# Optimization experiments

Measured on AMD Instinct MI355X. Metric: run time of the kernel, lower is better.

## Reference

```python
import jax, jax.numpy as jnp
import numpy as np

N_NODES = 50000
N_EDGES = 800000
DIM = 128
N_GRAPHS = 64
HEADS = 4
SCALE = (DIM // HEADS) ** -0.5
EPS = 1e-5
SLOPE = 0.01  # torch LeakyReLU default


def setup_inputs() -> dict:
    key = jax.random.key(0)
    ks = iter(jax.random.split(key, 48))
    def nrm(shape, s):
        return jax.random.normal(next(ks), shape, dtype=jnp.float32) * s
    inp = {
        "xA": nrm((N_NODES, DIM), 1.0),
        "xB": nrm((N_NODES, DIM), 1.0),
        "edge_index_A": jax.random.randint(next(ks), (2, N_EDGES), 0, N_NODES),
        "edge_index_B": jax.random.randint(next(ks), (2, N_EDGES), 0, N_NODES),
        # contiguous equal-size graph assignment (sorted, covers all B graphs)
        "batch_A": (jnp.arange(N_NODES) * N_GRAPHS) // N_NODES,
        "batch_B": (jnp.arange(N_NODES) * N_GRAPHS) // N_NODES,
    }
    s = DIM ** -0.5
    for name, shape in [("WA1", (DIM, DIM)), ("WA2", (DIM, DIM)),
                        ("WB1", (DIM, DIM)), ("WB2", (DIM, DIM)),
                        ("Wq", (DIM, DIM)), ("Wk", (DIM, DIM)),
                        ("Wv", (DIM, DIM)), ("Wo", (DIM, DIM)),
                        ("Wf1", (DIM, 2 * DIM)), ("Wf2", (2 * DIM, DIM)),
                        ("Wl1", (2 * DIM, DIM)), ("Wl2", (DIM, 1))]:
        inp[name] = nrm(shape, s)
    for name, shape in [("bA1", (DIM,)), ("bA2", (DIM,)), ("bB1", (DIM,)), ("bB2", (DIM,)),
                        ("bq", (DIM,)), ("bk", (DIM,)), ("bv", (DIM,)), ("bo", (DIM,)),
                        ("bf1", (2 * DIM,)), ("bf2", (DIM,)), ("bl1", (DIM,)), ("bl2", (1,))]:
        inp[name] = jnp.zeros(shape, jnp.float32)
    inp["g1"] = jnp.ones((DIM,), jnp.float32)
    inp["be1"] = jnp.zeros((DIM,), jnp.float32)
    inp["g2"] = jnp.ones((DIM,), jnp.float32)
    inp["be2"] = jnp.zeros((DIM,), jnp.float32)
    return inp


def _gcn(x, W, b, src, dst):
    # PyG GCNConv: XW, add self-loops, sym D^-1/2 (A+I) D^-1/2, scatter to dst, + bias
    h = x @ W
    deg = jax.ops.segment_sum(jnp.ones(src.shape, h.dtype), dst, N_NODES) + 1.0
    inv = jax.lax.rsqrt(deg)
    agg = jax.ops.segment_sum(h[src] * (inv[src] * inv[dst])[:, None], dst, N_NODES)
    return agg + h * (inv * inv)[:, None] + b  # self-loop term: norm_i^2 * h_i


def _encoder(x, edge_index, W1, b1, W2, b2):
    src, dst = edge_index[0], edge_index[1]
    h = jax.nn.leaky_relu(_gcn(x, W1, b1, src, dst), SLOPE)
    return _gcn(h, W2, b2, src, dst)  # dropout is identity in eval mode


def _pool(x, batch):
    s = jax.ops.segment_sum(x, batch, N_GRAPHS)
    c = jax.ops.segment_sum(jnp.ones((x.shape[0],), x.dtype), batch, N_GRAPHS)
    return s / c[:, None]


def _ln(x, g, b):
    m = x.mean(-1, keepdims=True)
    v = ((x - m) ** 2).mean(-1, keepdims=True)
    return (x - m) * jax.lax.rsqrt(v + EPS) * g + b


def reference(xA, xB, edge_index_A, edge_index_B, batch_A, batch_B,
              WA1, bA1, WA2, bA2, WB1, bB1, WB2, bB2,
              Wq, bq, Wk, bk, Wv, bv, Wo, bo,
              g1, be1, Wf1, bf1, Wf2, bf2, g2, be2,
              Wl1, bl1, Wl2, bl2):

    def cross(x_q, x_kv):
        Q = (x_q @ Wq + bq).reshape(-1, HEADS, DIM // HEADS)
        K = (x_kv @ Wk + bk).reshape(-1, HEADS, DIM // HEADS)
        V = (x_kv @ Wv + bv).reshape(-1, HEADS, DIM // HEADS)
        attn = jax.nn.softmax(jnp.einsum('qhd,khd->hqk', Q, K) * SCALE, axis=-1)
        out = jnp.einsum('hqk,khd->qhd', attn, V).reshape(x_q.shape[0], DIM)
        return out @ Wo + bo

    def block(x_q, x_kv):  # shared-weight CrossAttentionBlock (used both directions)
        x = _ln(x_q + cross(x_q, x_kv), g1, be1)
        ff = jax.nn.leaky_relu(x @ Wf1 + bf1, SLOPE) @ Wf2 + bf2
        return _ln(x + ff, g2, be2)

    gA = _encoder(xA, edge_index_A, WA1, bA1, WA2, bA2)
    gB = _encoder(xB, edge_index_B, WB1, bB1, WB2, bB2)
    hA = _pool(gA, batch_A)
    hB = _pool(gB, batch_B)
    hA_att = block(hA, hB)
    hB_att = block(hB, hA)
    h = jnp.concatenate([hA_att, hB_att], axis=-1)  # [B, 2*DIM]
    h = jax.nn.relu(h @ Wl1 + bl1)
    return h @ Wl2 + bl2  # [B, 1]
```

## Files before the change

### kernel.cpp

```cpp
#include <hip/hip_runtime.h>

#define N_NODESC 50000
#define N_EDGESC 800000
#define DIMC 128
#define NGC 64
#define HDC 32
#define SLOPEF 0.01f
#define EPSF 1e-5f
#define SCALEF 0.17677669529663687f

#define NBUK 782
#define KBLK 50
#define EPB 16000
#define GG 782
#define AG 12500

typedef __attribute__((ext_vector_type(8))) short bf16x8;
typedef __attribute__((ext_vector_type(4))) float f32x4;
typedef __attribute__((ext_vector_type(2))) float f32x2;

static __device__ __forceinline__ unsigned short f2bf(float f) {
  unsigned u = __float_as_uint(f);
  u = u + 0x7FFFu + ((u >> 16) & 1u);
  return (unsigned short)(u >> 16);
}
static __device__ __forceinline__ float bf2f(unsigned short h) {
  return __uint_as_float(((unsigned)h) << 16);
}

#if defined(__has_builtin)
#if __has_builtin(__builtin_amdgcn_cvt_pk_f32_fp8) && __has_builtin(__builtin_amdgcn_cvt_pk_fp8_f32)
#define HW_FP8 1
#endif
#endif
#ifndef HW_FP8
#define HW_FP8 0
#endif

static __device__ __forceinline__ unsigned enc_fp8(float x) {
  unsigned u = __float_as_uint(x);
  unsigned s = (u >> 24) & 0x80u;
  unsigned mag = u & 0x7FFFFFFFu;
  if (mag >= 0x43E00000u) return s | 0x7Eu;
  unsigned r = mag + 0x7FFFFu + ((mag >> 20) & 1u);
  int e8 = (int)(r >> 23) - 120;
  if (e8 <= 0) {
    float ax = __uint_as_float(mag);
    int m = (int)(ax * 512.0f + 0.5f);
    if (m > 7) m = 7;
    return s | (unsigned)m;
  }
  return s | ((unsigned)e8 << 3) | ((r >> 20) & 7u);
}
static __device__ __forceinline__ float dec_fp8(unsigned b) {
  unsigned em = b & 0x7Fu;
  float mag = (em >= 8) ? __uint_as_float((em << 20) + 0x3C000000u)
                        : (float)em * 0.001953125f;
  return (b & 0x80u) ? -mag : mag;
}
static __device__ __forceinline__ unsigned pk_fp8x4(float a, float b, float c, float d) {
#if HW_FP8
  int v = 0;
  v = __builtin_amdgcn_cvt_pk_fp8_f32(a, b, v, false);
  v = __builtin_amdgcn_cvt_pk_fp8_f32(c, d, v, true);
  return (unsigned)v;
#else
  return enc_fp8(a) | (enc_fp8(b) << 8) | (enc_fp8(c) << 16) | (enc_fp8(d) << 24);
#endif
}
static __device__ __forceinline__ float4 upk_fp8x4(unsigned v) {
#if HW_FP8
  f32x2 lo = __builtin_amdgcn_cvt_pk_f32_fp8((int)v, false);
  f32x2 hi = __builtin_amdgcn_cvt_pk_f32_fp8((int)v, true);
  return make_float4(lo[0], lo[1], hi[0], hi[1]);
#else
  return make_float4(dec_fp8(v & 0xFF), dec_fp8((v >> 8) & 0xFF),
                     dec_fp8((v >> 16) & 0xFF), dec_fp8(v >> 24));
#endif
}

__global__ __launch_bounds__(1024) void kbhist2(const int* __restrict__ eiA, const int* __restrict__ eiB,
                                                int* __restrict__ hist) {
  __shared__ int lh[NBUK];
  int side = blockIdx.x / KBLK, blk = blockIdx.x % KBLK;
  const int* ei = side ? eiB : eiA;
  int* hout = hist + side * KBLK * NBUK;
  int t = threadIdx.x;
  for (int i = t; i < NBUK; i += 1024) lh[i] = 0;
  __syncthreads();
  int e0 = blk * EPB;
  for (int e = e0 + t; e < e0 + EPB; e += 1024) {
    int d = ei[N_EDGESC + e];
    atomicAdd(&lh[d >> 6], 1);
  }
  __syncthreads();
  for (int i = t; i < NBUK; i += 1024) hout[blk * NBUK + i] = lh[i];
}

__global__ __launch_bounds__(1024) void kbscan2(const int* __restrict__ hist, int* __restrict__ bbase,
                                                int* __restrict__ bucket_base) {
  __shared__ int sd[1024];
  int side = blockIdx.x;
  const int* h = hist + side * KBLK * NBUK;
  int* bb = bbase + side * KBLK * NBUK;
  int* bub = bucket_base + side * (NBUK + 1);
  int t = threadIdx.x;
  int tot = 0;
  if (t < NBUK) {
    for (int k = 0; k < KBLK; ++k) tot += h[k * NBUK + t];
  }
  sd[t] = tot;
  __syncthreads();
  for (int off = 1; off < 1024; off <<= 1) {
    int u = (t >= off) ? sd[t - off] : 0;
    __syncthreads();
    sd[t] += u;
    __syncthreads();
  }
  if (t < NBUK) {
    int run = sd[t] - tot;
    bub[t] = run;
    for (int k = 0; k < KBLK; ++k) {
      bb[k * NBUK + t] = run;
      run += h[k * NBUK + t];
    }
  }
  if (t == 0) bub[NBUK] = N_EDGESC;
}

__global__ __launch_bounds__(1024) void kbin2(const int* __restrict__ eiA, const int* __restrict__ eiB,
                                              const int* __restrict__ bbase, unsigned* __restrict__ packed) {
  __shared__ int cur[NBUK];
  int side = blockIdx.x / KBLK, blk = blockIdx.x % KBLK;
  const int* ei = side ? eiB : eiA;
  const int* bb = bbase + side * KBLK * NBUK;
  unsigned* pk = packed + (size_t)side * N_EDGESC;
  int t = threadIdx.x;
  for (int i = t; i < NBUK; i += 1024) cur[i] = bb[blk * NBUK + i];
  __syncthreads();
  int e0 = blk * EPB;
  for (int e = e0 + t; e < e0 + EPB; e += 1024) {
    int s = ei[e];
    int d = ei[N_EDGESC + e];
    int b = d >> 6;
    int pos = atomicAdd(&cur[b], 1);
    pk[pos] = (unsigned)s | ((unsigned)(d & 63) << 16);
  }
}

__global__ __launch_bounds__(256) void kcsr2(const unsigned* __restrict__ packed, const int* __restrict__ bucket_base,
                                             unsigned short* __restrict__ csr16, int* __restrict__ rowptr,
                                             float* __restrict__ inv) {
  __shared__ int h64[64], o64[64], c64[64];
  int side = blockIdx.x / NBUK, b = blockIdx.x % NBUK;
  const unsigned* pk = packed + (size_t)side * N_EDGESC;
  const int* bub = bucket_base + side * (NBUK + 1);
  unsigned short* cs = csr16 + (size_t)side * N_EDGESC;
  int* rp = rowptr + side * (N_NODESC + 1);
  float* iv = inv + side * N_NODESC;
  int t = threadIdx.x;
  int beg = bub[b], end = bub[b + 1];
  if (t < 64) h64[t] = 0;
  __syncthreads();
  for (int e = beg + t; e < end; e += 256) atomicAdd(&h64[pk[e] >> 16], 1);
  __syncthreads();
  if (t == 0) {
    int run = 0;
    for (int j = 0; j < 64; ++j) { o64[j] = run; run += h64[j]; }
  }
  __syncthreads();
  if (t < 64) c64[t] = o64[t];
  __syncthreads();
  for (int e = beg + t; e < end; e += 256) {
    unsigned p = pk[e];
    int pos = atomicAdd(&c64[p >> 16], 1);
    cs[beg + pos] = (unsigned short)(p & 0xFFFFu);
  }
  if (t < 64) {
    int node = b * 64 + t;
    if (node < N_NODESC) {
      rp[node] = beg + o64[t];
      iv[node] = rsqrtf((float)h64[t] + 1.0f);
    }
  }
  if (b == NBUK - 1 && t == 0) rp[N_NODESC] = N_EDGESC;
}

__global__ __launch_bounds__(256) void wconv(const float* __restrict__ W0, const float* __restrict__ W1,
                                             const float* __restrict__ W2, const float* __restrict__ W3,
                                             unsigned short* __restrict__ Wt) {
  int m = blockIdx.x >> 4;
  int idx = (blockIdx.x & 15) * 256 + threadIdx.x;
  int fs = idx >> 6, lane = idx & 63;
  int ks = fs >> 3, nf = fs & 7;
  int n = nf * 16 + (lane & 15);
  int k0 = ks * 32 + (lane >> 4) * 8;
  const float* W = (m == 0) ? W0 : (m == 1) ? W1 : (m == 2) ? W2 : W3;
  unsigned short* hi = Wt + (size_t)m * 128 * 512 + (size_t)(fs * 2) * 512 + lane * 8;
  bf16x8 vh, vl;
#pragma unroll
  for (int j = 0; j < 8; ++j) {
    float a = W[(k0 + j) * DIMC + n];
    unsigned short h = f2bf(a);
    vh[j] = (short)h;
    vl[j] = (short)f2bf(a - bf2f(h));
  }
  *(bf16x8*)hi = vh;
  *(bf16x8*)(hi + 512) = vl;
}

static __device__ __forceinline__ void epi_store_fp8(const unsigned short* lds, unsigned* Y, int lb) {
  int tr = threadIdx.x >> 2, q = threadIdx.x & 3;
  int grow = lb * 64 + tr;
  if (grow >= N_NODESC) return;
#pragma unroll
  for (int i = 0; i < 8; ++i) {
    int col = (q + 4 * i) * 4;
    ushort4 v = *(const ushort4*)&lds[tr * 136 + col];
    unsigned pk = pk_fp8x4(bf2f(v.x), bf2f(v.y), bf2f(v.z), bf2f(v.w));
    Y[(size_t)grow * 32 + q + 4 * i] = pk;
  }
}

__global__ __launch_bounds__(256) void gemm_l1(const float* __restrict__ xA, const float* __restrict__ xB,
                                               const unsigned short* __restrict__ Wt, const float* __restrict__ inv,
                                               unsigned* __restrict__ H) {
  __shared__ unsigned short lds[64 * 136];
  int side = blockIdx.x / GG, lb = blockIdx.x % GG;
  const float* X = side ? xB : xA;
  const unsigned short* Wm = Wt + (size_t)(side * 2) * 128 * 512;
  const float* iv = inv + side * N_NODESC;
  unsigned* Y = H + (size_t)side * N_NODESC * 32;
  int wave = threadIdx.x >> 6, lane = threadIdx.x & 63;
  int l15 = lane & 15, kb = lane >> 4;
  int row0 = lb * 64 + wave * 16;
  int rA = row0 + l15;
  const bool valid = rA < N_NODESC;
  f32x4 acc[8];
#pragma unroll
  for (int nf = 0; nf < 8; ++nf) acc[nf] = 0.f;
#pragma unroll
  for (int ks = 0; ks < 4; ++ks) {
    int kbase = ks * 32 + kb * 8;
    bf16x8 a;
    if (valid) {
      const float* xp = &X[(size_t)rA * DIMC + kbase];
      float4 x0 = *(const float4*)xp;
      float4 x1 = *(const float4*)(xp + 4);
      a[0] = (short)f2bf(x0.x); a[1] = (short)f2bf(x0.y);
      a[2] = (short)f2bf(x0.z); a[3] = (short)f2bf(x0.w);
      a[4] = (short)f2bf(x1.x); a[5] = (short)f2bf(x1.y);
      a[6] = (short)f2bf(x1.z); a[7] = (short)f2bf(x1.w);
    } else {
      a = (short)0;
    }
    const unsigned short* wp = Wm + (size_t)(ks * 16) * 512 + lane * 8;
#pragma unroll
    for (int nf = 0; nf < 8; ++nf) {
      bf16x8 bh = *(const bf16x8*)(wp + (nf * 2) * 512);
      bf16x8 bl = *(const bf16x8*)(wp + (nf * 2 + 1) * 512);
      acc[nf] = __builtin_amdgcn_mfma_f32_16x16x32_bf16(a, bh, acc[nf], 0, 0, 0);
      acc[nf] = __builtin_amdgcn_mfma_f32_16x16x32_bf16(a, bl, acc[nf], 0, 0, 0);
    }
  }
  int lrow = wave * 16 + kb * 4;
#pragma unroll
  for (int r = 0; r < 4; ++r) {
    int rr = row0 + kb * 4 + r;
    float s = (rr < N_NODESC) ? iv[rr] * 16.0f : 0.f;
#pragma unroll
    for (int nf = 0; nf < 8; ++nf) {
      lds[(lrow + r) * 136 + nf * 16 + l15] = f2bf(acc[nf][r] * s);
    }
  }
  __syncthreads();
  epi_store_fp8(lds, Y, lb);
}

__global__ __launch_bounds__(256) void gemm_l2(const unsigned short* __restrict__ Gb,
                                               const unsigned short* __restrict__ Wt, const float* __restrict__ inv,
                                               unsigned* __restrict__ H) {
  __shared__ unsigned short lds[64 * 136];
  int side = blockIdx.x / GG, lb = blockIdx.x % GG;
  const unsigned short* X = Gb + (size_t)side * N_NODESC * DIMC;
  const unsigned short* Wm = Wt + (size_t)(side * 2 + 1) * 128 * 512;
  const float* iv = inv + side * N_NODESC;
  unsigned* Y = H + (size_t)side * N_NODESC * 32;
  int wave = threadIdx.x >> 6, lane = threadIdx.x & 63;
  int l15 = lane & 15, kb = lane >> 4;
  int row0 = lb * 64 + wave * 16;
  int rA = row0 + l15;
  const bool valid = rA < N_NODESC;
  f32x4 acc[8];
#pragma unroll
  for (int nf = 0; nf < 8; ++nf) acc[nf] = 0.f;
#pragma unroll
  for (int ks = 0; ks < 4; ++ks) {
    int kbase = ks * 32 + kb * 8;
    bf16x8 a;
    if (valid) {
      a = *(const bf16x8*)&X[(size_t)rA * DIMC + kbase];
    } else {
      a = (short)0;
    }
    const unsigned short* wp = Wm + (size_t)(ks * 16) * 512 + lane * 8;
#pragma unroll
    for (int nf = 0; nf < 8; ++nf) {
      bf16x8 bh = *(const bf16x8*)(wp + (nf * 2) * 512);
      bf16x8 bl = *(const bf16x8*)(wp + (nf * 2 + 1) * 512);
      acc[nf] = __builtin_amdgcn_mfma_f32_16x16x32_bf16(a, bh, acc[nf], 0, 0, 0);
      acc[nf] = __builtin_amdgcn_mfma_f32_16x16x32_bf16(a, bl, acc[nf], 0, 0, 0);
    }
  }
  int lrow = wave * 16 + kb * 4;
#pragma unroll
  for (int r = 0; r < 4; ++r) {
    int rr = row0 + kb * 4 + r;
    float s = (rr < N_NODESC) ? iv[rr] * 16.0f : 0.f;
#pragma unroll
    for (int nf = 0; nf < 8; ++nf) {
      lds[(lrow + r) * 136 + nf * 16 + l15] = f2bf(acc[nf][r] * s);
    }
  }
  __syncthreads();
  epi_store_fp8(lds, Y, lb);
}

__global__ __launch_bounds__(256) void agg12(const unsigned* __restrict__ H, const float* __restrict__ inv,
                                             const int* __restrict__ rowptr, const unsigned short* __restrict__ csr16,
                                             const float* __restrict__ biasA, const float* __restrict__ biasB,
                                             unsigned short* __restrict__ G, int do_relu) {
  int side = blockIdx.x / AG, lb = blockIdx.x % AG;
  int node = lb * 4 + (threadIdx.x >> 6);
  if (node >= N_NODESC) return;
  const unsigned* Hp = H + (size_t)side * N_NODESC * 32;
  const float* iv = inv + side * N_NODESC;
  const int* rp = rowptr + side * (N_NODESC + 1);
  const unsigned short* csr = csr16 + (size_t)side * N_EDGESC;
  const float* bias = side ? biasB : biasA;
  unsigned short* out = G + (size_t)side * N_NODESC * DIMC;
  int lane = threadIdx.x & 63;
  int ug = lane & 31;
  int slot = lane >> 5;
  int beg = rp[node], end = rp[node + 1];
  float4 acc = make_float4(0.f, 0.f, 0.f, 0.f);
  int e = beg;
  for (; e + 8 <= end; e += 8) {
    int s0 = csr[e + slot];
    int s1 = csr[e + 2 + slot];
    int s2 = csr[e + 4 + slot];
    int s3 = csr[e + 6 + slot];
    unsigned u0 = Hp[(size_t)s0 * 32 + ug];
    unsigned u1 = Hp[(size_t)s1 * 32 + ug];
    unsigned u2 = Hp[(size_t)s2 * 32 + ug];
    unsigned u3 = Hp[(size_t)s3 * 32 + ug];
    float4 v0 = upk_fp8x4(u0);
    float4 v1 = upk_fp8x4(u1);
    float4 v2 = upk_fp8x4(u2);
    float4 v3 = upk_fp8x4(u3);
    acc.x += (v0.x + v1.x) + (v2.x + v3.x);
    acc.y += (v0.y + v1.y) + (v2.y + v3.y);
    acc.z += (v0.z + v1.z) + (v2.z + v3.z);
    acc.w += (v0.w + v1.w) + (v2.w + v3.w);
  }
  for (int t = e + slot; t < end; t += 2) {
    int s = csr[t];
    float4 v = upk_fp8x4(Hp[(size_t)s * 32 + ug]);
    acc.x += v.x; acc.y += v.y; acc.z += v.z; acc.w += v.w;
  }
  acc.x += __shfl_xor(acc.x, 32, 64);
  acc.y += __shfl_xor(acc.y, 32, 64);
  acc.z += __shfl_xor(acc.z, 32, 64);
  acc.w += __shfl_xor(acc.w, 32, 64);
  if (slot == 0) {
    float4 sv = upk_fp8x4(Hp[(size_t)node * 32 + ug]);
    float sc = iv[node] * 0.0625f;
    const float* bp = &bias[ug * 4];
    float4 b = *(const float4*)bp;
    float4 o;
    o.x = (acc.x + sv.x) * sc + b.x;
    o.y = (acc.y + sv.y) * sc + b.y;
    o.z = (acc.z + sv.z) * sc + b.z;
    o.w = (acc.w + sv.w) * sc + b.w;
    if (do_relu) {
      o.x = (o.x > 0.f) ? o.x : SLOPEF * o.x;
      o.y = (o.y > 0.f) ? o.y : SLOPEF * o.y;
      o.z = (o.z > 0.f) ? o.z : SLOPEF * o.z;
      o.w = (o.w > 0.f) ? o.w : SLOPEF * o.w;
    }
    ushort4 ob;
    ob.x = f2bf(o.x); ob.y = f2bf(o.y); ob.z = f2bf(o.z); ob.w = f2bf(o.w);
    *(ushort4*)&out[(size_t)node * DIMC + ug * 4] = ob;
  }
}

__global__ __launch_bounds__(128) void pool2(const unsigned short* __restrict__ G,
                                             const int* __restrict__ batA, const int* __restrict__ batB,
                                             float* __restrict__ psA, float* __restrict__ psB,
                                             int* __restrict__ pcA, int* __restrict__ pcB) {
  int side = blockIdx.x / GG, lb = blockIdx.x % GG;
  const unsigned short* g = G + (size_t)side * N_NODESC * DIMC;
  const int* batch = side ? batB : batA;
  float* psum = side ? psB : psA;
  int* pcnt = side ? pcB : pcA;
  int t = threadIdx.x;
  int n0 = lb * 64;
  int nend = min(n0 + 64, N_NODESC);
  int cur = batch[n0];
  float acc = 0.f;
  int c = 0;
  for (int n = n0; n < nend; ++n) {
    int b = batch[n];
    if (b != cur) {
      atomicAdd(&psum[cur * DIMC + t], acc);
      if (t == 0) atomicAdd(&pcnt[cur], c);
      acc = 0.f;
      c = 0;
      cur = b;
    }
    acc += bf2f(g[(size_t)n * DIMC + t]);
    c += 1;
  }
  atomicAdd(&psum[cur * DIMC + t], acc);
  if (t == 0) atomicAdd(&pcnt[cur], c);
}

__global__ __launch_bounds__(128) void mean_kernel(const float* __restrict__ psA, const int* __restrict__ pcA,
                                                   const float* __restrict__ psB, const int* __restrict__ pcB,
                                                   float* __restrict__ hA, float* __restrict__ hB) {
  int dir = blockIdx.x >> 6, g = blockIdx.x & 63, t = threadIdx.x;
  const float* ps = dir ? psB : psA;
  const int* pc = dir ? pcB : pcA;
  float* h = dir ? hB : hA;
  h[g * DIMC + t] = ps[g * DIMC + t] / (float)max(pc[g], 1);
}

__global__ __launch_bounds__(128) void qkv_kernel(const float* __restrict__ hA, const float* __restrict__ hB,
                                                  const float* __restrict__ Wq, const float* __restrict__ bq,
                                                  const float* __restrict__ Wk, const float* __restrict__ bk,
                                                  const float* __restrict__ Wv, const float* __restrict__ bv,
                                                  float* __restrict__ Q0, float* __restrict__ K0, float* __restrict__ V0,
                                                  float* __restrict__ Q1, float* __restrict__ K1, float* __restrict__ V1) {
  __shared__ float xs[DIMC];
  int task = blockIdx.x >> 6, r = blockIdx.x & 63, t = threadIdx.x;
  const float *X, *W, *b;
  float* Y;
  switch (task) {
    case 0: X = hA; W = Wq; b = bq; Y = Q0; break;
    case 1: X = hB; W = Wk; b = bk; Y = K0; break;
    case 2: X = hB; W = Wv; b = bv; Y = V0; break;
    case 3: X = hB; W = Wq; b = bq; Y = Q1; break;
    case 4: X = hA; W = Wk; b = bk; Y = K1; break;
    default: X = hA; W = Wv; b = bv; Y = V1; break;
  }
  xs[t] = X[r * DIMC + t];
  __syncthreads();
  float acc = b[t];
  for (int k = 0; k < DIMC; ++k) acc += xs[k] * W[k * DIMC + t];
  Y[r * DIMC + t] = acc;
}

__global__ __launch_bounds__(64) void attn_kernel(const float* __restrict__ Q0, const float* __restrict__ K0,
                                                  const float* __restrict__ V0, const float* __restrict__ Q1,
                                                  const float* __restrict__ K1, const float* __restrict__ V1,
                                                  float* __restrict__ O0, float* __restrict__ O1) {
  __shared__ float ps[64];
  int b = blockIdx.x;
  int dir = b >> 8, h = (b >> 6) & 3, q = b & 63;
  const float* Q = dir ? Q1 : Q0;
  const float* K = dir ? K1 : K0;
  const float* V = dir ? V1 : V0;
  float* O = dir ? O1 : O0;
  int k = threadIdx.x;
  const float* qp = Q + q * DIMC + h * HDC;
  const float* kp = K + k * DIMC + h * HDC;
  float s = 0.f;
#pragma unroll
  for (int d = 0; d < HDC; ++d) s += qp[d] * kp[d];
  s *= SCALEF;
  float m = s;
#pragma unroll
  for (int off = 32; off >= 1; off >>= 1) m = fmaxf(m, __shfl_xor(m, off, 64));
  float p = __expf(s - m);
  float sum = p;
#pragma unroll
  for (int off = 32; off >= 1; off >>= 1) sum += __shfl_xor(sum, off, 64);
  p /= sum;
  ps[k] = p;
  __syncthreads();
  int half = k >> 5, d = k & 31;
  float acc = 0.f;
#pragma unroll
  for (int j = 0; j < 32; ++j) {
    int kk = half * 32 + j;
    acc += ps[kk] * V[kk * DIMC + h * HDC + d];
  }
  acc += __shfl_xor(acc, 32, 64);
  if (half == 0) O[q * DIMC + h * HDC + d] = acc;
}

__device__ inline float blk_sum128(float v, float* red) {
#pragma unroll
  for (int off = 32; off >= 1; off >>= 1) v += __shfl_xor(v, off, 64);
  if ((threadIdx.x & 63) == 0) red[threadIdx.x >> 6] = v;
  __syncthreads();
  float r = red[0] + red[1];
  __syncthreads();
  return r;
}

__global__ __launch_bounds__(128) void oln_kernel(const float* __restrict__ O0, const float* __restrict__ O1,
                                                  const float* __restrict__ hA, const float* __restrict__ hB,
                                                  const float* __restrict__ Wo, const float* __restrict__ bo,
                                                  const float* __restrict__ g1, const float* __restrict__ be1,
                                                  float* __restrict__ X0, float* __restrict__ X1) {
  __shared__ float os[DIMC];
  __shared__ float red[2];
  int dir = blockIdx.x >> 6, q = blockIdx.x & 63, t = threadIdx.x;
  const float* O = dir ? O1 : O0;
  const float* xq = dir ? hB : hA;
  float* Xo = dir ? X1 : X0;
  os[t] = O[q * DIMC + t];
  __syncthreads();
  float acc = bo[t] + xq[q * DIMC + t];
  for (int k = 0; k < DIMC; ++k) acc += os[k] * Wo[k * DIMC + t];
  float mean = blk_sum128(acc, red) * (1.f / DIMC);
  float d = acc - mean;
  float var = blk_sum128(d * d, red) * (1.f / DIMC);
  Xo[q * DIMC + t] = d * rsqrtf(var + EPSF) * g1[t] + be1[t];
}

__global__ __launch_bounds__(256) void ff1_kernel(const float* __restrict__ X0, const float* __restrict__ X1,
                                                  const float* __restrict__ Wf1, const float* __restrict__ bf1,
                                                  float* __restrict__ F0, float* __restrict__ F1) {
  __shared__ float xs[DIMC];
  int dir = blockIdx.x >> 6, q = blockIdx.x & 63, t = threadIdx.x;
  const float* X = dir ? X1 : X0;
  float* F = dir ? F1 : F0;
  if (t < DIMC) xs[t] = X[q * DIMC + t];
  __syncthreads();
  float acc = bf1[t];
  for (int k = 0; k < DIMC; ++k) acc += xs[k] * Wf1[k * 256 + t];
  acc = (acc > 0.f) ? acc : SLOPEF * acc;
  F[q * 256 + t] = acc;
}

__global__ __launch_bounds__(128) void ffln_kernel(const float* __restrict__ F0, const float* __restrict__ F1,
                                                   const float* __restrict__ X0, const float* __restrict__ X1,
                                                   const float* __restrict__ Wf2, const float* __restrict__ bf2,
                                                   const float* __restrict__ g2, const float* __restrict__ be2,
                                                   float* __restrict__ Y0, float* __restrict__ Y1) {
  __shared__ float fs[256];
  __shared__ float red[2];
  int dir = blockIdx.x >> 6, q = blockIdx.x & 63, t = threadIdx.x;
  const float* F = dir ? F1 : F0;
  const float* X = dir ? X1 : X0;
  float* Y = dir ? Y1 : Y0;
  fs[t] = F[q * 256 + t];
  fs[t + 128] = F[q * 256 + t + 128];
  __syncthreads();
  float acc = bf2[t] + X[q * DIMC + t];
  for (int k = 0; k < 256; ++k) acc += fs[k] * Wf2[k * DIMC + t];
  float mean = blk_sum128(acc, red) * (1.f / DIMC);
  float d = acc - mean;
  float var = blk_sum128(d * d, red) * (1.f / DIMC);
  Y[q * DIMC + t] = d * rsqrtf(var + EPSF) * g2[t] + be2[t];
}

__global__ __launch_bounds__(128) void head_kernel(const float* __restrict__ Y0, const float* __restrict__ Y1,
                                                   const float* __restrict__ Wl1, const float* __restrict__ bl1,
                                                   const float* __restrict__ Wl2, const float* __restrict__ bl2,
                                                   float* __restrict__ out) {
  __shared__ float cs[256];
  __shared__ float red[2];
  int g = blockIdx.x, t = threadIdx.x;
  cs[t] = Y0[g * DIMC + t];
  cs[t + 128] = Y1[g * DIMC + t];
  __syncthreads();
  float acc = bl1[t];
  for (int k = 0; k < 256; ++k) acc += cs[k] * Wl1[k * DIMC + t];
  acc = fmaxf(acc, 0.f);
  float s = blk_sum128(acc * Wl2[t], red);
  if (t == 0) out[g] = s + bl2[0];
}

extern "C" void kernel_launch(void* const* d_in, const int* in_sizes, int n_in,
                              void* d_out, int out_size, void* d_ws, size_t ws_size,
                              hipStream_t stream) {
  const float* xA = (const float*)d_in[0];
  const float* xB = (const float*)d_in[1];
  const int* eiA = (const int*)d_in[2];
  const int* eiB = (const int*)d_in[3];
  const int* batA = (const int*)d_in[4];
  const int* batB = (const int*)d_in[5];
  const float* WA1 = (const float*)d_in[6];
  const float* WA2 = (const float*)d_in[7];
  const float* WB1 = (const float*)d_in[8];
  const float* WB2 = (const float*)d_in[9];
  const float* Wq = (const float*)d_in[10];
  const float* Wk = (const float*)d_in[11];
  const float* Wv = (const float*)d_in[12];
  const float* Wo = (const float*)d_in[13];
  const float* Wf1 = (const float*)d_in[14];
  const float* Wf2 = (const float*)d_in[15];
  const float* Wl1 = (const float*)d_in[16];
  const float* Wl2 = (const float*)d_in[17];
  const float* bA1 = (const float*)d_in[18];
  const float* bA2 = (const float*)d_in[19];
  const float* bB1 = (const float*)d_in[20];
  const float* bB2 = (const float*)d_in[21];
  const float* bq = (const float*)d_in[22];
  const float* bk = (const float*)d_in[23];
  const float* bv = (const float*)d_in[24];
  const float* bo = (const float*)d_in[25];
  const float* bf1 = (const float*)d_in[26];
  const float* bf2 = (const float*)d_in[27];
  const float* bl1 = (const float*)d_in[28];
  const float* bl2 = (const float*)d_in[29];
  const float* g1 = (const float*)d_in[30];
  const float* be1 = (const float*)d_in[31];
  const float* g2 = (const float*)d_in[32];
  const float* be2 = (const float*)d_in[33];

  char* base = (char*)d_ws;
  size_t off = 0;
  auto alloc = [&](size_t bytes) -> char* {
    char* r = base + off;
    off += (bytes + 255) & ~(size_t)255;
    return r;
  };
  unsigned* h_buf = (unsigned*)alloc((size_t)2 * N_NODESC * 32 * 4);
  unsigned short* g_buf = (unsigned short*)alloc((size_t)2 * N_NODESC * DIMC * 2);
  unsigned* packed = (unsigned*)alloc((size_t)2 * N_EDGESC * 4);
  unsigned short* csr16 = (unsigned short*)alloc((size_t)2 * N_EDGESC * 2);
  int* rowptr = (int*)alloc((size_t)2 * (N_NODESC + 1) * 4);
  float* inv = (float*)alloc((size_t)2 * N_NODESC * 4);
  int* hist = (int*)alloc((size_t)2 * KBLK * NBUK * 4);
  int* bbase = (int*)alloc((size_t)2 * KBLK * NBUK * 4);
  int* bucket_base = (int*)alloc((size_t)2 * (NBUK + 1) * 4);
  unsigned short* wtbuf = (unsigned short*)alloc((size_t)4 * 128 * 512 * 2);
  size_t poff0 = off;
  float* psA = (float*)alloc(NGC * DIMC * 4);
  float* psB = (float*)alloc(NGC * DIMC * 4);
  int* pcA = (int*)alloc(NGC * 4);
  int* pcB = (int*)alloc(NGC * 4);
  size_t pbytes = off - poff0;
  float* mhA = (float*)alloc(NGC * DIMC * 4);
  float* mhB = (float*)alloc(NGC * DIMC * 4);
  float* Q0 = (float*)alloc(NGC * DIMC * 4);
  float* K0 = (float*)alloc(NGC * DIMC * 4);
  float* V0 = (float*)alloc(NGC * DIMC * 4);
  float* Q1 = (float*)alloc(NGC * DIMC * 4);
  float* K1 = (float*)alloc(NGC * DIMC * 4);
  float* V1 = (float*)alloc(NGC * DIMC * 4);
  float* O0 = (float*)alloc(NGC * DIMC * 4);
  float* O1 = (float*)alloc(NGC * DIMC * 4);
  float* X0 = (float*)alloc(NGC * DIMC * 4);
  float* X1 = (float*)alloc(NGC * DIMC * 4);
  float* F0 = (float*)alloc(NGC * 256 * 4);
  float* F1 = (float*)alloc(NGC * 256 * 4);
  float* Y0 = (float*)alloc(NGC * DIMC * 4);
  float* Y1 = (float*)alloc(NGC * DIMC * 4);

  hipMemsetAsync(base + poff0, 0, pbytes, stream);
  wconv<<<64, 256, 0, stream>>>(WA1, WA2, WB1, WB2, wtbuf);

  kbhist2<<<2 * KBLK, 1024, 0, stream>>>(eiA, eiB, hist);
  kbscan2<<<2, 1024, 0, stream>>>(hist, bbase, bucket_base);
  kbin2<<<2 * KBLK, 1024, 0, stream>>>(eiA, eiB, bbase, packed);
  kcsr2<<<2 * NBUK, 256, 0, stream>>>(packed, bucket_base, csr16, rowptr, inv);

  gemm_l1<<<2 * GG, 256, 0, stream>>>(xA, xB, wtbuf, inv, h_buf);
  agg12<<<2 * AG, 256, 0, stream>>>(h_buf, inv, rowptr, csr16, bA1, bB1, g_buf, 1);
  gemm_l2<<<2 * GG, 256, 0, stream>>>(g_buf, wtbuf, inv, h_buf);
  agg12<<<2 * AG, 256, 0, stream>>>(h_buf, inv, rowptr, csr16, bA2, bB2, g_buf, 0);
  pool2<<<2 * GG, 128, 0, stream>>>(g_buf, batA, batB, psA, psB, pcA, pcB);

  mean_kernel<<<128, 128, 0, stream>>>(psA, pcA, psB, pcB, mhA, mhB);
  qkv_kernel<<<384, 128, 0, stream>>>(mhA, mhB, Wq, bq, Wk, bk, Wv, bv, Q0, K0, V0, Q1, K1, V1);
  attn_kernel<<<512, 64, 0, stream>>>(Q0, K0, V0, Q1, K1, V1, O0, O1);
  oln_kernel<<<128, 128, 0, stream>>>(O0, O1, mhA, mhB, Wo, bo, g1, be1, X0, X1);
  ff1_kernel<<<128, 256, 0, stream>>>(X0, X1, Wf1, bf1, F0, F1);
  ffln_kernel<<<128, 128, 0, stream>>>(F0, F1, X0, X1, Wf2, bf2, g2, be2, Y0, Y1);
  head_kernel<<<64, 128, 0, stream>>>(Y0, Y1, Wl1, bl1, Wl2, bl2, (float*)d_out);
}
```

Measured before the change: 268.0 us.

## Widen aggregation loads to 8 bytes and fuse tail kernels

The GCN aggregation kernel now has each lane read a uint2 (8 fp8 values). Sixteen lanes cover one feature row, so four edges are gathered in parallel per wave, with a 16-edge unrolled loop and a two-step shuffle reduction. Separately, the small post-pool kernels are merged: mean with QKV, output projection/LN with FF1, and FF2/LN with the head. This cuts three launches and their global round-trips. The trade-off is more accumulator registers in the aggregation and a 256-thread block where half the threads idle during the Wo stage.

```diff
diff --git a/kernel.cpp b/kernel.cpp
--- a/kernel.cpp
+++ b/kernel.cpp
@@ -326,6 +326,13 @@
   epi_store_fp8(lds, Y, lb);
 }
 
+static __device__ __forceinline__ void addu2(float* acc, uint2 u) {
+  float4 a = upk_fp8x4(u.x);
+  float4 b = upk_fp8x4(u.y);
+  acc[0] += a.x; acc[1] += a.y; acc[2] += a.z; acc[3] += a.w;
+  acc[4] += b.x; acc[5] += b.y; acc[6] += b.z; acc[7] += b.w;
+}
+
 __global__ __launch_bounds__(256) void agg12(const unsigned* __restrict__ H, const float* __restrict__ inv,
                                              const int* __restrict__ rowptr, const unsigned short* __restrict__ csr16,
                                              const float* __restrict__ biasA, const float* __restrict__ biasB,
@@ -340,57 +347,60 @@
   const float* bias = side ? biasB : biasA;
   unsigned short* out = G + (size_t)side * N_NODESC * DIMC;
   int lane = threadIdx.x & 63;
-  int ug = lane & 31;
-  int slot = lane >> 5;
+  int g16 = lane & 15;
+  int ug2 = g16 * 2;
+  int slot = lane >> 4;
   int beg = rp[node], end = rp[node + 1];
-  float4 acc = make_float4(0.f, 0.f, 0.f, 0.f);
+  float acc[8];
+#pragma unroll
+  for (int j = 0; j < 8; ++j) acc[j] = 0.f;
   int e = beg;
-  for (; e + 8 <= end; e += 8) {
+  for (; e + 16 <= end; e += 16) {
     int s0 = csr[e + slot];
-    int s1 = csr[e + 2 + slot];
-    int s2 = csr[e + 4 + slot];
-    int s3 = csr[e + 6 + slot];
-    unsigned u0 = Hp[(size_t)s0 * 32 + ug];
-    unsigned u1 = Hp[(size_t)s1 * 32 + ug];
-    unsigned u2 = Hp[(size_t)s2 * 32 + ug];
-    unsigned u3 = Hp[(size_t)s3 * 32 + ug];
-    float4 v0 = upk_fp8x4(u0);
-    float4 v1 = upk_fp8x4(u1);
-    float4 v2 = upk_fp8x4(u2);
-    float4 v3 = upk_fp8x4(u3);
-    acc.x += (v0.x + v1.x) + (v2.x + v3.x);
-    acc.y += (v0.y + v1.y) + (v2.y + v3.y);
-    acc.z += (v0.z + v1.z) + (v2.z + v3.z);
-    acc.w += (v0.w + v1.w) + (v2.w + v3.w);
-  }
-  for (int t = e + slot; t < end; t += 2) {
-    int s = csr[t];
-    float4 v = upk_fp8x4(Hp[(size_t)s * 32 + ug]);
-    acc.x += v.x; acc.y += v.y; acc.z += v.z; acc.w += v.w;
-  }
-  acc.x += __shfl_xor(acc.x, 32, 64);
-  acc.y += __shfl_xor(acc.y, 32, 64);
-  acc.z += __shfl_xor(acc.z, 32, 64);
-  acc.w += __shfl_xor(acc.w, 32, 64);
+    int s1 = csr[e + 4 + slot];
+    int s2 = csr[e + 8 + slot];
+    int s3 = csr[e + 12 + slot];
+    uint2 u0 = *(const uint2*)&Hp[(size_t)s0 * 32 + ug2];
+    uint2 u1 = *(const uint2*)&Hp[(size_t)s1 * 32 + ug2];
+    uint2 u2 = *(const uint2*)&Hp[(size_t)s2 * 32 + ug2];
+    uint2 u3 = *(const uint2*)&Hp[(size_t)s3 * 32 + ug2];
+    addu2(acc, u0); addu2(acc, u1); addu2(acc, u2); addu2(acc, u3);
+  }
+  for (int t2 = e + slot; t2 < end; t2 += 4) {
+    uint2 u = *(const uint2*)&Hp[(size_t)csr[t2] * 32 + ug2];
+    addu2(acc, u);
+  }
+#pragma unroll
+  for (int j = 0; j < 8; ++j) {
+    acc[j] += __shfl_xor(acc[j], 16, 64);
+    acc[j] += __shfl_xor(acc[j], 32, 64);
+  }
   if (slot == 0) {
-    float4 sv = upk_fp8x4(Hp[(size_t)node * 32 + ug]);
+    uint2 su = *(const uint2*)&Hp[(size_t)node * 32 + ug2];
+    float4 sa = upk_fp8x4(su.x);
+    float4 sb = upk_fp8x4(su.y);
     float sc = iv[node] * 0.0625f;
-    const float* bp = &bias[ug * 4];
-    float4 b = *(const float4*)bp;
-    float4 o;
-    o.x = (acc.x + sv.x) * sc + b.x;
-    o.y = (acc.y + sv.y) * sc + b.y;
-    o.z = (acc.z + sv.z) * sc + b.z;
-    o.w = (acc.w + sv.w) * sc + b.w;
+    float4 b0 = *(const float4*)&bias[g16 * 8];
+    float4 b1 = *(const float4*)&bias[g16 * 8 + 4];
+    float o[8];
+    o[0] = (acc[0] + sa.x) * sc + b0.x;
+    o[1] = (acc[1] + sa.y) * sc + b0.y;
+    o[2] = (acc[2] + sa.z) * sc + b0.z;
+    o[3] = (acc[3] + sa.w) * sc + b0.w;
+    o[4] = (acc[4] + sb.x) * sc + b1.x;
+    o[5] = (acc[5] + sb.y) * sc + b1.y;
+    o[6] = (acc[6] + sb.z) * sc + b1.z;
+    o[7] = (acc[7] + sb.w) * sc + b1.w;
     if (do_relu) {
-      o.x = (o.x > 0.f) ? o.x : SLOPEF * o.x;
-      o.y = (o.y > 0.f) ? o.y : SLOPEF * o.y;
-      o.z = (o.z > 0.f) ? o.z : SLOPEF * o.z;
-      o.w = (o.w > 0.f) ? o.w : SLOPEF * o.w;
-    }
-    ushort4 ob;
-    ob.x = f2bf(o.x); ob.y = f2bf(o.y); ob.z = f2bf(o.z); ob.w = f2bf(o.w);
-    *(ushort4*)&out[(size_t)node * DIMC + ug * 4] = ob;
+#pragma unroll
+      for (int j = 0; j < 8; ++j) o[j] = (o[j] > 0.f) ? o[j] : SLOPEF * o[j];
+    }
+    uint4 w;
+    w.x = (unsigned)f2bf(o[0]) | ((unsigned)f2bf(o[1]) << 16);
+    w.y = (unsigned)f2bf(o[2]) | ((unsigned)f2bf(o[3]) << 16);
+    w.z = (unsigned)f2bf(o[4]) | ((unsigned)f2bf(o[5]) << 16);
+    w.w = (unsigned)f2bf(o[6]) | ((unsigned)f2bf(o[7]) << 16);
+    *(uint4*)&out[(size_t)node * DIMC + g16 * 8] = w;
   }
 }
 
@@ -425,35 +435,33 @@
   if (t == 0) atomicAdd(&pcnt[cur], c);
 }
 
-__global__ __launch_bounds__(128) void mean_kernel(const float* __restrict__ psA, const int* __restrict__ pcA,
-                                                   const float* __restrict__ psB, const int* __restrict__ pcB,
-                                                   float* __restrict__ hA, float* __restrict__ hB) {
-  int dir = blockIdx.x >> 6, g = blockIdx.x & 63, t = threadIdx.x;
-  const float* ps = dir ? psB : psA;
-  const int* pc = dir ? pcB : pcA;
-  float* h = dir ? hB : hA;
-  h[g * DIMC + t] = ps[g * DIMC + t] / (float)max(pc[g], 1);
-}
-
-__global__ __launch_bounds__(128) void qkv_kernel(const float* __restrict__ hA, const float* __restrict__ hB,
-                                                  const float* __restrict__ Wq, const float* __restrict__ bq,
-                                                  const float* __restrict__ Wk, const float* __restrict__ bk,
-                                                  const float* __restrict__ Wv, const float* __restrict__ bv,
-                                                  float* __restrict__ Q0, float* __restrict__ K0, float* __restrict__ V0,
-                                                  float* __restrict__ Q1, float* __restrict__ K1, float* __restrict__ V1) {
+__global__ __launch_bounds__(128) void meanqkv(const float* __restrict__ psA, const int* __restrict__ pcA,
+                                               const float* __restrict__ psB, const int* __restrict__ pcB,
+                                               const float* __restrict__ Wq, const float* __restrict__ bq,
+                                               const float* __restrict__ Wk, const float* __restrict__ bk,
+                                               const float* __restrict__ Wv, const float* __restrict__ bv,
+                                               float* __restrict__ mhA, float* __restrict__ mhB,
+                                               float* __restrict__ Q0, float* __restrict__ K0, float* __restrict__ V0,
+                                               float* __restrict__ Q1, float* __restrict__ K1, float* __restrict__ V1) {
   __shared__ float xs[DIMC];
   int task = blockIdx.x >> 6, r = blockIdx.x & 63, t = threadIdx.x;
-  const float *X, *W, *b;
+  bool sideA = (task == 0 || task == 4 || task == 5);
+  const float* ps = sideA ? psA : psB;
+  const int* pc = sideA ? pcA : pcB;
+  const float *W, *b;
   float* Y;
   switch (task) {
-    case 0: X = hA; W = Wq; b = bq; Y = Q0; break;
-    case 1: X = hB; W = Wk; b = bk; Y = K0; break;
-    case 2: X = hB; W = Wv; b = bv; Y = V0; break;
-    case 3: X = hB; W = Wq; b = bq; Y = Q1; break;
-    case 4: X = hA; W = Wk; b = bk; Y = K1; break;
-    default: X = hA; W = Wv; b = bv; Y = V1; break;
-  }
-  xs[t] = X[r * DIMC + t];
+    case 0: W = Wq; b = bq; Y = Q0; break;
+    case 1: W = Wk; b = bk; Y = K0; break;
+    case 2: W = Wv; b = bv; Y = V0; break;
+    case 3: W = Wq; b = bq; Y = Q1; break;
+    case 4: W = Wk; b = bk; Y = K1; break;
+    default: W = Wv; b = bv; Y = V1; break;
+  }
+  float xv = ps[r * DIMC + t] / (float)max(pc[r], 1);
+  xs[t] = xv;
+  if (task == 0) mhA[r * DIMC + t] = xv;
+  if (task == 3) mhB[r * DIMC + t] = xv;
   __syncthreads();
   float acc = b[t];
   for (int k = 0; k < DIMC; ++k) acc += xs[k] * W[k * DIMC + t];
@@ -509,74 +517,80 @@
   return r;
 }
 
-__global__ __launch_bounds__(128) void oln_kernel(const float* __restrict__ O0, const float* __restrict__ O1,
-                                                  const float* __restrict__ hA, const float* __restrict__ hB,
-                                                  const float* __restrict__ Wo, const float* __restrict__ bo,
-                                                  const float* __restrict__ g1, const float* __restrict__ be1,
-                                                  float* __restrict__ X0, float* __restrict__ X1) {
+__global__ __launch_bounds__(256) void olnff1(const float* __restrict__ O0, const float* __restrict__ O1,
+                                              const float* __restrict__ mhA, const float* __restrict__ mhB,
+                                              const float* __restrict__ Wo, const float* __restrict__ bo,
+                                              const float* __restrict__ g1, const float* __restrict__ be1,
+                                              const float* __restrict__ Wf1, const float* __restrict__ bf1,
+                                              float* __restrict__ X0, float* __restrict__ X1,
+                                              float* __restrict__ F0, float* __restrict__ F1) {
   __shared__ float os[DIMC];
-  __shared__ float red[2];
+  __shared__ float xs[DIMC];
+  __shared__ float red4[4];
   int dir = blockIdx.x >> 6, q = blockIdx.x & 63, t = threadIdx.x;
   const float* O = dir ? O1 : O0;
-  const float* xq = dir ? hB : hA;
+  const float* xq = dir ? mhB : mhA;
   float* Xo = dir ? X1 : X0;
-  os[t] = O[q * DIMC + t];
-  __syncthreads();
-  float acc = bo[t] + xq[q * DIMC + t];
-  for (int k = 0; k < DIMC; ++k) acc += os[k] * Wo[k * DIMC + t];
-  float mean = blk_sum128(acc, red) * (1.f / DIMC);
-  float d = acc - mean;
-  float var = blk_sum128(d * d, red) * (1.f / DIMC);
-  Xo[q * DIMC + t] = d * rsqrtf(var + EPSF) * g1[t] + be1[t];
-}
-
-__global__ __launch_bounds__(256) void ff1_kernel(const float* __restrict__ X0, const float* __restrict__ X1,
-                                                  const float* __restrict__ Wf1, const float* __restrict__ bf1,
-                                                  float* __restrict__ F0, float* __restrict__ F1) {
-  __shared__ float xs[DIMC];
-  int dir = blockIdx.x >> 6, q = blockIdx.x & 63, t = threadIdx.x;
-  const float* X = dir ? X1 : X0;
   float* F = dir ? F1 : F0;
-  if (t < DIMC) xs[t] = X[q * DIMC + t];
-  __syncthreads();
-  float acc = bf1[t];
-  for (int k = 0; k < DIMC; ++k) acc += xs[k] * Wf1[k * 256 + t];
-  acc = (acc > 0.f) ? acc : SLOPEF * acc;
-  F[q * 256 + t] = acc;
-}
-
-__global__ __launch_bounds__(128) void ffln_kernel(const float* __restrict__ F0, const float* __restrict__ F1,
-                                                   const float* __restrict__ X0, const float* __restrict__ X1,
-                                                   const float* __restrict__ Wf2, const float* __restrict__ bf2,
-                                                   const float* __restrict__ g2, const float* __restrict__ be2,
-                                                   float* __restrict__ Y0, float* __restrict__ Y1) {
+  if (t < DIMC) os[t] = O[q * DIMC + t];
+  __syncthreads();
+  bool act = t < DIMC;
+  float acc = 0.f;
+  if (act) {
+    acc = bo[t] + xq[q * DIMC + t];
+    for (int k = 0; k < DIMC; ++k) acc += os[k] * Wo[k * DIMC + t];
+  }
+  float v = act ? acc : 0.f;
+#pragma unroll
+  for (int off = 32; off >= 1; off >>= 1) v += __shfl_xor(v, off, 64);
+  if ((t & 63) == 0) red4[t >> 6] = v;
+  __syncthreads();
+  float mean = (red4[0] + red4[1] + red4[2] + red4[3]) * (1.f / DIMC);
+  __syncthreads();
+  float d = act ? (acc - mean) : 0.f;
+  float v2 = d * d;
+#pragma unroll
+  for (int off = 32; off >= 1; off >>= 1) v2 += __shfl_xor(v2, off, 64);
+  if ((t & 63) == 0) red4[t >> 6] = v2;
+  __syncthreads();
+  float var = (red4[0] + red4[1] + red4[2] + red4[3]) * (1.f / DIMC);
+  if (act) {
+    float xv = d * rsqrtf(var + EPSF) * g1[t] + be1[t];
+    xs[t] = xv;
+    Xo[q * DIMC + t] = xv;
+  }
+  __syncthreads();
+  float facc = bf1[t];
+  for (int k = 0; k < DIMC; ++k) facc += xs[k] * Wf1[k * 256 + t];
+  facc = (facc > 0.f) ? facc : SLOPEF * facc;
+  F[q * 256 + t] = facc;
+}
+
+__global__ __launch_bounds__(128) void fflnhead(const float* __restrict__ F0, const float* __restrict__ F1,
+                                                const float* __restrict__ X0, const float* __restrict__ X1,
+                                                const float* __restrict__ Wf2, const float* __restrict__ bf2,
+                                                const float* __restrict__ g2, const float* __restrict__ be2,
+                                                const float* __restrict__ Wl1, const float* __restrict__ bl1,
+                                                const float* __restrict__ Wl2, const float* __restrict__ bl2,
+                                                float* __restrict__ out) {
   __shared__ float fs[256];
-  __shared__ float red[2];
-  int dir = blockIdx.x >> 6, q = blockIdx.x & 63, t = threadIdx.x;
-  const float* F = dir ? F1 : F0;
-  const float* X = dir ? X1 : X0;
-  float* Y = dir ? Y1 : Y0;
-  fs[t] = F[q * 256 + t];
-  fs[t + 128] = F[q * 256 + t + 128];
-  __syncthreads();
-  float acc = bf2[t] + X[q * DIMC + t];
-  for (int k = 0; k < 256; ++k) acc += fs[k] * Wf2[k * DIMC + t];
-  float mean = blk_sum128(acc, red) * (1.f / DIMC);
-  float d = acc - mean;
-  float var = blk_sum128(d * d, red) * (1.f / DIMC);
-  Y[q * DIMC + t] = d * rsqrtf(var + EPSF) * g2[t] + be2[t];
-}
-
-__global__ __launch_bounds__(128) void head_kernel(const float* __restrict__ Y0, const float* __restrict__ Y1,
-                                                   const float* __restrict__ Wl1, const float* __restrict__ bl1,
-                                                   const float* __restrict__ Wl2, const float* __restrict__ bl2,
-                                                   float* __restrict__ out) {
   __shared__ float cs[256];
   __shared__ float red[2];
   int g = blockIdx.x, t = threadIdx.x;
-  cs[t] = Y0[g * DIMC + t];
-  cs[t + 128] = Y1[g * DIMC + t];
-  __syncthreads();
+  for (int dir = 0; dir < 2; ++dir) {
+    const float* F = dir ? F1 : F0;
+    const float* X = dir ? X1 : X0;
+    fs[t] = F[g * 256 + t];
+    fs[t + 128] = F[g * 256 + t + 128];
+    __syncthreads();
+    float acc = bf2[t] + X[g * DIMC + t];
+    for (int k = 0; k < 256; ++k) acc += fs[k] * Wf2[k * DIMC + t];
+    float mean = blk_sum128(acc, red) * (1.f / DIMC);
+    float d = acc - mean;
+    float var = blk_sum128(d * d, red) * (1.f / DIMC);
+    cs[dir * DIMC + t] = d * rsqrtf(var + EPSF) * g2[t] + be2[t];
+    __syncthreads();
+  }
   float acc = bl1[t];
   for (int k = 0; k < 256; ++k) acc += cs[k] * Wl1[k * DIMC + t];
   acc = fmaxf(acc, 0.f);
@@ -659,8 +673,6 @@
   float* X1 = (float*)alloc(NGC * DIMC * 4);
   float* F0 = (float*)alloc(NGC * 256 * 4);
   float* F1 = (float*)alloc(NGC * 256 * 4);
-  float* Y0 = (float*)alloc(NGC * DIMC * 4);
-  float* Y1 = (float*)alloc(NGC * DIMC * 4);
 
   hipMemsetAsync(base + poff0, 0, pbytes, stream);
   wconv<<<64, 256, 0, stream>>>(WA1, WA2, WB1, WB2, wtbuf);
@@ -676,11 +688,9 @@
   agg12<<<2 * AG, 256, 0, stream>>>(h_buf, inv, rowptr, csr16, bA2, bB2, g_buf, 0);
   pool2<<<2 * GG, 128, 0, stream>>>(g_buf, batA, batB, psA, psB, pcA, pcB);
 
-  mean_kernel<<<128, 128, 0, stream>>>(psA, pcA, psB, pcB, mhA, mhB);
-  qkv_kernel<<<384, 128, 0, stream>>>(mhA, mhB, Wq, bq, Wk, bk, Wv, bv, Q0, K0, V0, Q1, K1, V1);
+  meanqkv<<<384, 128, 0, stream>>>(psA, pcA, psB, pcB, Wq, bq, Wk, bk, Wv, bv,
+                                   mhA, mhB, Q0, K0, V0, Q1, K1, V1);
   attn_kernel<<<512, 64, 0, stream>>>(Q0, K0, V0, Q1, K1, V1, O0, O1);
-  oln_kernel<<<128, 128, 0, stream>>>(O0, O1, mhA, mhB, Wo, bo, g1, be1, X0, X1);
-  ff1_kernel<<<128, 256, 0, stream>>>(X0, X1, Wf1, bf1, F0, F1);
-  ffln_kernel<<<128, 128, 0, stream>>>(F0, F1, X0, X1, Wf2, bf2, g2, be2, Y0, Y1);
-  head_kernel<<<64, 128, 0, stream>>>(Y0, Y1, Wl1, bl1, Wl2, bl2, (float*)d_out);
-}
+  olnff1<<<128, 256, 0, stream>>>(O0, O1, mhA, mhB, Wo, bo, g1, be1, Wf1, bf1, X0, X1, F0, F1);
+  fflnhead<<<64, 128, 0, stream>>>(F0, F1, X0, X1, Wf2, bf2, g2, be2, Wl1, bl1, Wl2, bl2, (float*)d_out);
+}
```

After: 262.5 us. -2.1%, faster.
